# Kernel optimization log

Hardware: AMD Instinct MI355X
Metric: run time of the kernel (lower is better)

Reference implementation:

```python
import jax, jax.numpy as jnp
import numpy as np

N = 50000
E = 800000
IN_CH = 256
OUT_CH = 64   # per-head channels (PyG out_channels)
HEADS = 4
NEG_SLOPE = 0.2


def setup_inputs() -> dict:
    key = jax.random.key(0)
    k = jax.random.split(key, 8)
    x = jax.random.normal(k[0], (N, IN_CH), dtype=jnp.float32)
    edge_index = jax.random.randint(k[1], (2, E), 0, N, dtype=jnp.int64)
    # GATConv parameters
    W = jax.random.normal(k[2], (IN_CH, HEADS * OUT_CH), dtype=jnp.float32) * (1.0 / np.sqrt(IN_CH))
    att_src = jax.random.normal(k[3], (HEADS, OUT_CH), dtype=jnp.float32) * 0.1
    att_dst = jax.random.normal(k[4], (HEADS, OUT_CH), dtype=jnp.float32) * 0.1
    bias = jnp.zeros((OUT_CH,), dtype=jnp.float32)
    # residual linear (bias=False)
    W_res = jax.random.normal(k[5], (IN_CH, OUT_CH), dtype=jnp.float32) * (1.0 / np.sqrt(IN_CH))
    return {"x": x, "edge_index": edge_index, "W": W, "att_src": att_src,
            "att_dst": att_dst, "bias": bias, "W_res": W_res}


def _gat_forward(x, edge_index, W, att_src, att_dst, bias, W_res):
    # residual branch
    x_res = x @ W_res                                   # [N, OUT_CH]

    # node transform: [N, H, C]
    xw = (x @ W).reshape(N, HEADS, OUT_CH)
    # per-node attention logits, [N, H]
    a_src = jnp.einsum('nhc,hc->nh', xw, att_src)
    a_dst = jnp.einsum('nhc,hc->nh', xw, att_dst)

    # add self-loops (PyG GATConv default add_self_loops=True)
    loops = jnp.arange(N, dtype=edge_index.dtype)
    src = jnp.concatenate([edge_index[0], loops])       # [E+N]
    dst = jnp.concatenate([edge_index[1], loops])       # [E+N]

    # per-edge logits + leaky relu, [E+N, H]
    alpha = jax.nn.leaky_relu(a_src[src] + a_dst[dst], NEG_SLOPE)

    # segment softmax over destination nodes
    m = jax.ops.segment_max(alpha, dst, num_segments=N)    # [N, H]
    e = jnp.exp(alpha - m[dst])
    denom = jax.ops.segment_sum(e, dst, num_segments=N)    # [N, H]
    a = e / denom[dst]                                     # [E+N, H]
    # (dropout p=0.1 on attention coeffs is identity in eval mode)

    # weighted scatter-aggregate: [N, H, C]
    msgs = xw[src] * a[:, :, None]
    out = jax.ops.segment_sum(msgs, dst, num_segments=N)

    # concat=False -> mean over heads, then bias
    x_conv = out.mean(axis=1) + bias                     # [N, OUT_CH]
    return jax.nn.relu(x_conv + x_res)


def reference(x, edge_index, W, att_src, att_dst, bias, W_res):
    return _gat_forward(x, edge_index, W, att_src, att_dst, bias, W_res)
```

## Files before the change

### kernel.cpp

```cpp
#include <hip/hip_runtime.h>
#include <math.h>

#define N_NODES 50000
#define N_EDGES 800000
#define IN_CH   256
#define OUT_CH  64
#define HEADS   4
#define NEG_SLOPE 0.2f
#define NCOLS   320
#define NTILES  20
#define NKK     8
#define PACK_BLOCKS 40
#define GEMM_BLOCKS 782
#define NBINS   391
#define P1_BLOCKS 256
#define EPB     3125
#define AGG_BLOCKS 6250
#define STASH_CAP 2816

typedef __attribute__((ext_vector_type(8))) short short8;
typedef __attribute__((ext_vector_type(4))) float f32x4;

__device__ __forceinline__ float lrelu(float v) {
    return v > 0.f ? v : NEG_SLOPE * v;
}
__device__ __forceinline__ unsigned bf16_rne(float f) {
    unsigned u = __float_as_uint(f);
    return (u + 0x7FFFu + ((u >> 16) & 1u)) >> 16;
}
__device__ __forceinline__ unsigned pack2(float lo, float hi) {
    return bf16_rne(lo) | (bf16_rne(hi) << 16);
}
__device__ __forceinline__ float bflo(unsigned u) { return __uint_as_float(u << 16); }
__device__ __forceinline__ float bfhi(unsigned u) { return __uint_as_float(u & 0xFFFF0000u); }
__device__ __forceinline__ short8 as_short8(uint4 u) {
    union { uint4 u4; short8 s8; } cv; cv.u4 = u; return cv.s8;
}

__global__ __launch_bounds__(256) void pack_B(
    const float* __restrict__ W, const float* __restrict__ Wres,
    uint4* __restrict__ Bp)
{
    const int idx  = blockIdx.x * 256 + threadIdx.x;
    const int kk   = idx / (NTILES * 64);
    const int rem  = idx - kk * (NTILES * 64);
    const int t    = rem >> 6;
    const int lane = rem & 63;
    const int colL = lane & 15, quad = lane >> 4;
    const int col  = t * 16 + colL;
    const int k0   = kk * 32 + quad * 8;
    float v[8];
    #pragma unroll
    for (int j = 0; j < 8; ++j) {
        const int k = k0 + j;
        v[j] = (col < IN_CH) ? W[(size_t)k * IN_CH + col]
                             : Wres[(size_t)k * OUT_CH + (col - IN_CH)];
    }
    uint4 u;
    u.x = pack2(v[0], v[1]); u.y = pack2(v[2], v[3]);
    u.z = pack2(v[4], v[5]); u.w = pack2(v[6], v[7]);
    Bp[(kk * NTILES + t) * 64 + lane] = u;
}

__global__ __launch_bounds__(256) void gemm_hist(
    const float* __restrict__ x, const uint4* __restrict__ Bp,
    uint2* __restrict__ xw2, float* __restrict__ xres,
    const int* __restrict__ ei, int* __restrict__ M,
    const float* __restrict__ attS, const float* __restrict__ attD,
    float* __restrict__ asrc, float* __restrict__ adst)
{
    __shared__ uint4 Alds[4 * NKK * 64];
    __shared__ float logS[64][HEADS];
    __shared__ float logD[64][HEADS];

    if (blockIdx.x >= GEMM_BLOCKS) {
        const int blk = blockIdx.x - GEMM_BLOCKS;
        int* lh = (int*)Alds;
        for (int b = threadIdx.x; b < NBINS; b += 256) lh[b] = 0;
        __syncthreads();
        const int e0 = blk * EPB;
        #pragma unroll
        for (int r = 0; r < 13; ++r) {
            const int idx = (r << 8) + threadIdx.x;
            if (idx < EPB)
                atomicAdd(&lh[ei[N_EDGES + e0 + idx] >> 7], 1);
        }
        __syncthreads();
        for (int b = threadIdx.x; b < NBINS; b += 256)
            M[(size_t)b * P1_BLOCKS + blk] = lh[b];
        return;
    }

    const int tid = threadIdx.x;
    const int n0  = blockIdx.x * 64;

    logS[tid >> 2][tid & 3] = 0.f;
    logD[tid >> 2][tid & 3] = 0.f;

    #pragma unroll
    for (int i = 0; i < 8; ++i) {
        const int e    = i * 256 + tid;
        const int g    = e >> 9;
        const int kk   = (e >> 6) & 7;
        const int lane = e & 63;
        const int cL   = lane & 15, qd = lane >> 4;
        const int row  = n0 + g * 16 + cL;
        const int k0   = kk * 32 + qd * 8;
        uint4 u = make_uint4(0u, 0u, 0u, 0u);
        if (row < N_NODES) {
            const float4 a = *reinterpret_cast<const float4*>(x + (size_t)row * IN_CH + k0);
            const float4 b = *reinterpret_cast<const float4*>(x + (size_t)row * IN_CH + k0 + 4);
            u.x = pack2(a.x, a.y); u.y = pack2(a.z, a.w);
            u.z = pack2(b.x, b.y); u.w = pack2(b.z, b.w);
        }
        Alds[(g * NKK + kk) * 64 + lane] = u;
    }
    __syncthreads();

    const int lane = tid & 63;
    const int wv   = tid >> 6;
    const int colL = lane & 15, quad = lane >> 4;

    f32x4 acc[4][5];
    #pragma unroll
    for (int rg = 0; rg < 4; ++rg)
        #pragma unroll
        for (int j = 0; j < 5; ++j) acc[rg][j] = (f32x4){0.f, 0.f, 0.f, 0.f};

    for (int kk = 0; kk < NKK; ++kk) {
        uint4 bu[5];
        #pragma unroll
        for (int j = 0; j < 5; ++j)
            bu[j] = Bp[(kk * NTILES + j * 4 + wv) * 64 + lane];
        #pragma unroll
        for (int rg = 0; rg < 4; ++rg) {
            const short8 a = as_short8(Alds[(rg * NKK + kk) * 64 + lane]);
            #pragma unroll
            for (int j = 0; j < 5; ++j)
                acc[rg][j] = __builtin_amdgcn_mfma_f32_16x16x32_bf16(
                    a, as_short8(bu[j]), acc[rg][j], 0, 0, 0);
        }
    }

    #pragma unroll
    for (int rg = 0; rg < 4; ++rg) {
        #pragma unroll
        for (int r = 0; r < 4; ++r) {
            const int row = n0 + rg * 16 + quad * 4 + r;
            if (row < N_NODES) {
                xw2[(size_t)row * 64 + wv * 16 + colL] = make_uint2(
                    pack2(acc[rg][0][r], acc[rg][1][r]),
                    pack2(acc[rg][2][r], acc[rg][3][r]));
                xres[(size_t)row * OUT_CH + wv * 16 + colL] = acc[rg][4][r];
            }
        }
    }

    float aSr[HEADS], aDr[HEADS];
    #pragma unroll
    for (int h = 0; h < HEADS; ++h) {
        aSr[h] = attS[h * 64 + wv * 16 + colL];
        aDr[h] = attD[h * 64 + wv * 16 + colL];
    }
    #pragma unroll
    for (int rg = 0; rg < 4; ++rg) {
        #pragma unroll
        for (int h = 0; h < HEADS; ++h) {
            #pragma unroll
            for (int r = 0; r < 4; ++r) {
                float vS = acc[rg][h][r] * aSr[h];
                float vD = acc[rg][h][r] * aDr[h];
                #pragma unroll
                for (int m = 1; m < 16; m <<= 1) {
                    vS += __shfl_xor(vS, m);
                    vD += __shfl_xor(vD, m);
                }
                if (colL == 0) {
                    atomicAdd(&logS[rg * 16 + quad * 4 + r][h], vS);
                    atomicAdd(&logD[rg * 16 + quad * 4 + r][h], vD);
                }
            }
        }
    }
    __syncthreads();
    {
        const int rl = tid >> 2, h = tid & 3;
        const int row = n0 + rl;
        if (row < N_NODES) {
            asrc[(size_t)row * HEADS + h] = logS[rl][h];
            adst[(size_t)row * HEADS + h] = logD[rl][h];
        }
    }
}

__global__ __launch_bounds__(256) void binscan_M(
    int* __restrict__ M, int* __restrict__ binCnt)
{
    __shared__ int ws[4];
    const int t = threadIdx.x, lane = t & 63, w = t >> 6;
    const int b = blockIdx.x;
    const int v = M[(size_t)b * P1_BLOCKS + t];
    int sc = v;
    #pragma unroll
    for (int off = 1; off < 64; off <<= 1) {
        const int n = __shfl_up(sc, off);
        if (lane >= off) sc += n;
    }
    if (lane == 63) ws[w] = sc;
    __syncthreads();
    int prefix = 0;
    for (int j = 0; j < w; ++j) prefix += ws[j];
    M[(size_t)b * P1_BLOCKS + t] = prefix + sc - v;
    if (t == 255) binCnt[b] = prefix + sc;
}

__global__ __launch_bounds__(256) void part_mid(
    const int* __restrict__ ei, const int* __restrict__ M,
    const int* __restrict__ binCnt, unsigned* __restrict__ mid)
{
    __shared__ int bc[NBINS];
    __shared__ int bs[NBINS];
    __shared__ int baseL[NBINS];
    __shared__ int lh[NBINS];
    __shared__ int ws[4];
    const int t = threadIdx.x, lane = t & 63, wv = t >> 6;
    const int blk = blockIdx.x;

    for (int b = t; b < NBINS; b += 256) {
        bc[b] = binCnt[b];
        baseL[b] = M[(size_t)b * P1_BLOCKS + blk];
        lh[b] = 0;
    }
    __syncthreads();

    int tot0;
    {
        const int v = bc[t];
        int sc = v;
        #pragma unroll
        for (int off = 1; off < 64; off <<= 1) {
            const int n = __shfl_up(sc, off);
            if (lane >= off) sc += n;
        }
        if (lane == 63) ws[wv] = sc;
        __syncthreads();
        int prefix = 0;
        for (int j = 0; j < wv; ++j) prefix += ws[j];
        bs[t] = prefix + sc - v;
        tot0 = ws[0] + ws[1] + ws[2] + ws[3];
        __syncthreads();
    }
    {
        const int i2 = 256 + t;
        const int v = (i2 < NBINS) ? bc[i2] : 0;
        int sc = v;
        #pragma unroll
        for (int off = 1; off < 64; off <<= 1) {
            const int n = __shfl_up(sc, off);
            if (lane >= off) sc += n;
        }
        if (lane == 63) ws[wv] = sc;
        __syncthreads();
        int prefix = 0;
        for (int j = 0; j < wv; ++j) prefix += ws[j];
        if (i2 < NBINS) bs[i2] = tot0 + prefix + sc - v;
        __syncthreads();
    }
    for (int b = t; b < NBINS; b += 256) baseL[b] += bs[b];
    __syncthreads();

    const int e0 = blk * EPB;
    #pragma unroll
    for (int r = 0; r < 13; ++r) {
        const int idx = (r << 8) + t;
        if (idx < EPB) {
            const int e = e0 + idx;
            const int d = ei[N_EDGES + e];
            const int b = d >> 7;
            const int pos = atomicAdd(&lh[b], 1);
            mid[baseL[b] + pos] = ((unsigned)(d & 127) << 17) | (unsigned)ei[e];
        }
    }
}

__global__ __launch_bounds__(256) void scatter_fine2(
    const unsigned* __restrict__ mid, const int* __restrict__ binCnt,
    int* __restrict__ cnt, int* __restrict__ lscan, int* __restrict__ esrc)
{
    __shared__ int ws[4];
    __shared__ int c128[128];
    __shared__ int o128[128];
    __shared__ int w0tot;
    __shared__ unsigned stash[STASH_CAP];
    const int t = threadIdx.x, lane = t & 63, wv = t >> 6;
    const int b = blockIdx.x;

    int acc = 0;
    for (int j = t; j < NBINS; j += 256)
        if (j < b) acc += binCnt[j];
    #pragma unroll
    for (int off = 32; off >= 1; off >>= 1) acc += __shfl_xor(acc, off);
    if (lane == 0) ws[wv] = acc;
    if (t < 128) c128[t] = 0;
    __syncthreads();
    const int base = ws[0] + ws[1] + ws[2] + ws[3];
    const int n = binCnt[b];

    for (int i = t; i < n; i += 256) {
        const unsigned m = mid[base + i];
        if (i < STASH_CAP) stash[i] = m;
        atomicAdd(&c128[m >> 17], 1);
    }
    __syncthreads();

    if (t < 128) {
        const int v = c128[t];
        int sc = v;
        #pragma unroll
        for (int off = 1; off < 64; off <<= 1) {
            const int nn = __shfl_up(sc, off);
            if (lane >= off) sc += nn;
        }
        if (t == 63) w0tot = sc;
        __syncthreads();
        const int ex = sc - v + (t >= 64 ? w0tot : 0);
        o128[t] = ex;
        const int d = (b << 7) + t;
        if (d < N_NODES) {
            cnt[d] = v;
            lscan[d] = base + ex;
        }
        c128[t] = 0;
    } else {
        __syncthreads();
    }
    __syncthreads();

    for (int i = t; i < n; i += 256) {
        const unsigned m = (i < STASH_CAP) ? stash[i] : mid[base + i];
        const int dlo = (int)(m >> 17);
        const int pos = atomicAdd(&c128[dlo], 1);
        esrc[base + o128[dlo] + pos] = (int)(m & 0x1FFFFu);
    }
}

__global__ __launch_bounds__(256) void aggregate(
    const int* __restrict__ esrc, const int* __restrict__ lscan,
    const int* __restrict__ cnt,
    const float* __restrict__ asrc, const float* __restrict__ adst,
    const uint2* __restrict__ xw2, const float* __restrict__ xres,
    const float* __restrict__ bias, float* __restrict__ out,
    const int d0)
{
    __shared__ float4 wbuf[4][64];
    __shared__ int    sbuf[4][64];
    const int t = threadIdx.x;
    const int lane = t & 63;
    const int wv   = t >> 6;

    const int d = d0 + blockIdx.x * 4 + wv;
    const int row = lscan[d];
    const int deg = cnt[d];
    const float4 ad = *reinterpret_cast<const float4*>(adst + (size_t)d * 4);
    const char* xwB = (const char*)xw2;
    const int laneB = lane << 3;

    float dn0 = 0.f, dn1 = 0.f, dn2 = 0.f, dn3 = 0.f;
    float ac0 = 0.f, ac1 = 0.f, ac2 = 0.f, ac3 = 0.f;

    for (int base = 0; base < deg; base += 64) {
        const int m = min(64, deg - base);
        if (lane < m) {
            const int s = esrc[row + base + lane];
            const float4 as = *reinterpret_cast<const float4*>(asrc + (size_t)s * 4);
            const float e0 = __expf(lrelu(as.x + ad.x));
            const float e1 = __expf(lrelu(as.y + ad.y));
            const float e2 = __expf(lrelu(as.z + ad.z));
            const float e3 = __expf(lrelu(as.w + ad.w));
            dn0 += e0; dn1 += e1; dn2 += e2; dn3 += e3;
            wbuf[wv][lane] = make_float4(e0, e1, e2, e3);
            sbuf[wv][lane] = s << 9;
        }
        int j = 0;
        for (; j + 4 <= m; j += 4) {
            uint2 v0 = *(const uint2*)(xwB + sbuf[wv][j]     + laneB);
            uint2 v1 = *(const uint2*)(xwB + sbuf[wv][j + 1] + laneB);
            uint2 v2 = *(const uint2*)(xwB + sbuf[wv][j + 2] + laneB);
            uint2 v3 = *(const uint2*)(xwB + sbuf[wv][j + 3] + laneB);
            {
                const float4 w = wbuf[wv][j];
                ac0 = fmaf(w.x, bflo(v0.x), ac0); ac1 = fmaf(w.y, bfhi(v0.x), ac1);
                ac2 = fmaf(w.z, bflo(v0.y), ac2); ac3 = fmaf(w.w, bfhi(v0.y), ac3);
            }
            {
                const float4 w = wbuf[wv][j + 1];
                ac0 = fmaf(w.x, bflo(v1.x), ac0); ac1 = fmaf(w.y, bfhi(v1.x), ac1);
                ac2 = fmaf(w.z, bflo(v1.y), ac2); ac3 = fmaf(w.w, bfhi(v1.y), ac3);
            }
            {
                const float4 w = wbuf[wv][j + 2];
                ac0 = fmaf(w.x, bflo(v2.x), ac0); ac1 = fmaf(w.y, bfhi(v2.x), ac1);
                ac2 = fmaf(w.z, bflo(v2.y), ac2); ac3 = fmaf(w.w, bfhi(v2.y), ac3);
            }
            {
                const float4 w = wbuf[wv][j + 3];
                ac0 = fmaf(w.x, bflo(v3.x), ac0); ac1 = fmaf(w.y, bfhi(v3.x), ac1);
                ac2 = fmaf(w.z, bflo(v3.y), ac2); ac3 = fmaf(w.w, bfhi(v3.y), ac3);
            }
        }
        for (; j < m; ++j) {
            const float4 w = wbuf[wv][j];
            const uint2 v = *(const uint2*)(xwB + sbuf[wv][j] + laneB);
            ac0 = fmaf(w.x, bflo(v.x), ac0);
            ac1 = fmaf(w.y, bfhi(v.x), ac1);
            ac2 = fmaf(w.z, bflo(v.y), ac2);
            ac3 = fmaf(w.w, bfhi(v.y), ac3);
        }
    }

    #pragma unroll
    for (int off = 32; off >= 1; off >>= 1) {
        dn0 += __shfl_xor(dn0, off);
        dn1 += __shfl_xor(dn1, off);
        dn2 += __shfl_xor(dn2, off);
        dn3 += __shfl_xor(dn3, off);
    }
    const float4 asd = *reinterpret_cast<const float4*>(asrc + (size_t)d * 4);
    const float s0 = __expf(lrelu(asd.x + ad.x));
    const float s1 = __expf(lrelu(asd.y + ad.y));
    const float s2 = __expf(lrelu(asd.z + ad.z));
    const float s3 = __expf(lrelu(asd.w + ad.w));
    const uint2 u = xw2[(size_t)d * 64 + lane];
    ac0 = fmaf(s0, bflo(u.x), ac0); ac1 = fmaf(s1, bfhi(u.x), ac1);
    ac2 = fmaf(s2, bflo(u.y), ac2); ac3 = fmaf(s3, bfhi(u.y), ac3);
    const float i0 = 0.25f / (dn0 + s0);
    const float i1 = 0.25f / (dn1 + s1);
    const float i2 = 0.25f / (dn2 + s2);
    const float i3 = 0.25f / (dn3 + s3);
    const float v = ac0 * i0 + ac1 * i1 + ac2 * i2 + ac3 * i3
                  + bias[lane] + xres[(size_t)d * OUT_CH + lane];
    out[(size_t)d * OUT_CH + lane] = fmaxf(v, 0.f);
}

extern "C" void kernel_launch(void* const* d_in, const int* in_sizes, int n_in,
                              void* d_out, int out_size, void* d_ws, size_t ws_size,
                              hipStream_t stream) {
    const float* x    = (const float*)d_in[0];
    const int*   ei   = (const int*)d_in[1];
    const float* W    = (const float*)d_in[2];
    const float* attS = (const float*)d_in[3];
    const float* attD = (const float*)d_in[4];
    const float* bias = (const float*)d_in[5];
    const float* Wres = (const float*)d_in[6];
    float* out = (float*)d_out;

    char* p = (char*)d_ws;
    uint4*    Bp      = (uint4*)p;    p += (size_t)NKK * NTILES * 64 * 16;
    uint2*    xw2     = (uint2*)p;    p += (size_t)N_NODES * 64 * 8;
    float*    xres    = (float*)p;    p += (size_t)N_NODES * OUT_CH * 4;
    float*    asrc    = (float*)p;    p += (size_t)N_NODES * HEADS * 4;
    float*    adst    = (float*)p;    p += (size_t)N_NODES * HEADS * 4;
    int*      M       = (int*)p;      p += (size_t)NBINS * P1_BLOCKS * 4;
    int*      binCnt  = (int*)p;      p += 512 * 4;
    int*      cnt     = (int*)p;      p += (size_t)N_NODES * 4;
    int*      lscan   = (int*)p;      p += (size_t)N_NODES * 4;
    unsigned* mid     = (unsigned*)p; p += (size_t)N_EDGES * 4;
    int*      esrc    = (int*)p;      p += (size_t)N_EDGES * 4;

    pack_B<<<PACK_BLOCKS, 256, 0, stream>>>(W, Wres, Bp);
    gemm_hist<<<GEMM_BLOCKS + P1_BLOCKS, 256, 0, stream>>>(
        x, Bp, xw2, xres, ei, M, attS, attD, asrc, adst);
    binscan_M<<<NBINS, 256, 0, stream>>>(M, binCnt);
    part_mid<<<P1_BLOCKS, 256, 0, stream>>>(ei, M, binCnt, mid);
    scatter_fine2<<<NBINS, 256, 0, stream>>>(mid, binCnt, cnt, lscan, esrc);
    aggregate<<<AGG_BLOCKS, 256, 0, stream>>>(
        esrc, lscan, cnt, asrc, adst, xw2, xres, bias, out, 0);
    aggregate<<<AGG_BLOCKS, 256, 0, stream>>>(
        esrc, lscan, cnt, asrc, adst, xw2, xres, bias, out, 25000);
}
```

Measured before the change: 237.5 us.

## Restructure GEMM so each wave owns 16 rows across all 320 columns

The fused GEMM previously staged a 64-row bf16 A tile in LDS and split the 320 output columns across waves, so attention logits had to be combined through shared-memory atomics after a barrier. Now each wave loads its own 16 rows of x straight from global memory into registers and computes all 20 column tiles. That removes the LDS staging, both block barriers and the shared atomics, and lets the asrc/adst logits be written as float4 after in-wave shuffles. The cost is 80 accumulator registers per lane and each wave re-reading all of B from global or L2. Separately, the two half-sized aggregate launches become one launch covering all 50000 nodes.

```diff
diff --git a/kernel.cpp b/kernel.cpp
--- a/kernel.cpp
+++ b/kernel.cpp
@@ -15,7 +15,7 @@
 #define NBINS   391
 #define P1_BLOCKS 256
 #define EPB     3125
-#define AGG_BLOCKS 6250
+#define AGG_BLOCKS 12500
 #define STASH_CAP 2816
 
 typedef __attribute__((ext_vector_type(8))) short short8;
@@ -69,13 +69,10 @@
     const float* __restrict__ attS, const float* __restrict__ attD,
     float* __restrict__ asrc, float* __restrict__ adst)
 {
-    __shared__ uint4 Alds[4 * NKK * 64];
-    __shared__ float logS[64][HEADS];
-    __shared__ float logD[64][HEADS];
+    __shared__ int lh[NBINS];
 
     if (blockIdx.x >= GEMM_BLOCKS) {
         const int blk = blockIdx.x - GEMM_BLOCKS;
-        int* lh = (int*)Alds;
         for (int b = threadIdx.x; b < NBINS; b += 256) lh[b] = 0;
         __syncthreads();
         const int e0 = blk * EPB;
@@ -91,104 +88,90 @@
         return;
     }
 
-    const int tid = threadIdx.x;
-    const int n0  = blockIdx.x * 64;
-
-    logS[tid >> 2][tid & 3] = 0.f;
-    logD[tid >> 2][tid & 3] = 0.f;
-
-    #pragma unroll
-    for (int i = 0; i < 8; ++i) {
-        const int e    = i * 256 + tid;
-        const int g    = e >> 9;
-        const int kk   = (e >> 6) & 7;
-        const int lane = e & 63;
-        const int cL   = lane & 15, qd = lane >> 4;
-        const int row  = n0 + g * 16 + cL;
-        const int k0   = kk * 32 + qd * 8;
-        uint4 u = make_uint4(0u, 0u, 0u, 0u);
-        if (row < N_NODES) {
-            const float4 a = *reinterpret_cast<const float4*>(x + (size_t)row * IN_CH + k0);
-            const float4 b = *reinterpret_cast<const float4*>(x + (size_t)row * IN_CH + k0 + 4);
-            u.x = pack2(a.x, a.y); u.y = pack2(a.z, a.w);
-            u.z = pack2(b.x, b.y); u.w = pack2(b.z, b.w);
-        }
-        Alds[(g * NKK + kk) * 64 + lane] = u;
-    }
-    __syncthreads();
-
+    const int tid  = threadIdx.x;
     const int lane = tid & 63;
     const int wv   = tid >> 6;
-    const int colL = lane & 15, quad = lane >> 4;
-
-    f32x4 acc[4][5];
-    #pragma unroll
-    for (int rg = 0; rg < 4; ++rg)
-        #pragma unroll
-        for (int j = 0; j < 5; ++j) acc[rg][j] = (f32x4){0.f, 0.f, 0.f, 0.f};
+    const int cL   = lane & 15, qd = lane >> 4;
+    const int n0   = blockIdx.x * 64;
+    const int arow = n0 + wv * 16 + cL;
+    const bool rowOK = arow < N_NODES;
+    const float* xrow = x + (size_t)arow * IN_CH + qd * 8;
+
+    f32x4 acc[NTILES];
+    #pragma unroll
+    for (int j = 0; j < NTILES; ++j) acc[j] = (f32x4){0.f, 0.f, 0.f, 0.f};
 
     for (int kk = 0; kk < NKK; ++kk) {
-        uint4 bu[5];
-        #pragma unroll
-        for (int j = 0; j < 5; ++j)
-            bu[j] = Bp[(kk * NTILES + j * 4 + wv) * 64 + lane];
-        #pragma unroll
-        for (int rg = 0; rg < 4; ++rg) {
-            const short8 a = as_short8(Alds[(rg * NKK + kk) * 64 + lane]);
+        uint4 a = make_uint4(0u, 0u, 0u, 0u);
+        if (rowOK) {
+            const float4 p = *reinterpret_cast<const float4*>(xrow + kk * 32);
+            const float4 q = *reinterpret_cast<const float4*>(xrow + kk * 32 + 4);
+            a.x = pack2(p.x, p.y); a.y = pack2(p.z, p.w);
+            a.z = pack2(q.x, q.y); a.w = pack2(q.z, q.w);
+        }
+        const short8 af = as_short8(a);
+        #pragma unroll
+        for (int jc = 0; jc < 5; ++jc) {
+            uint4 bu[4];
             #pragma unroll
-            for (int j = 0; j < 5; ++j)
-                acc[rg][j] = __builtin_amdgcn_mfma_f32_16x16x32_bf16(
-                    a, as_short8(bu[j]), acc[rg][j], 0, 0, 0);
-        }
-    }
-
-    #pragma unroll
-    for (int rg = 0; rg < 4; ++rg) {
-        #pragma unroll
-        for (int r = 0; r < 4; ++r) {
-            const int row = n0 + rg * 16 + quad * 4 + r;
-            if (row < N_NODES) {
-                xw2[(size_t)row * 64 + wv * 16 + colL] = make_uint2(
-                    pack2(acc[rg][0][r], acc[rg][1][r]),
-                    pack2(acc[rg][2][r], acc[rg][3][r]));
-                xres[(size_t)row * OUT_CH + wv * 16 + colL] = acc[rg][4][r];
-            }
-        }
-    }
-
-    float aSr[HEADS], aDr[HEADS];
+            for (int u = 0; u < 4; ++u)
+                bu[u] = Bp[(kk * NTILES + jc * 4 + u) * 64 + lane];
+            #pragma unroll
+            for (int u = 0; u < 4; ++u)
+                acc[jc * 4 + u] = __builtin_amdgcn_mfma_f32_16x16x32_bf16(
+                    af, as_short8(bu[u]), acc[jc * 4 + u], 0, 0, 0);
+        }
+    }
+
+    float vS[16], vD[16];
+    #pragma unroll
+    for (int i = 0; i < 16; ++i) { vS[i] = 0.f; vD[i] = 0.f; }
     #pragma unroll
     for (int h = 0; h < HEADS; ++h) {
-        aSr[h] = attS[h * 64 + wv * 16 + colL];
-        aDr[h] = attD[h * 64 + wv * 16 + colL];
-    }
-    #pragma unroll
-    for (int rg = 0; rg < 4; ++rg) {
-        #pragma unroll
-        for (int h = 0; h < HEADS; ++h) {
+        #pragma unroll
+        for (int s = 0; s < 4; ++s) {
+            const float aSv = attS[h * 64 + s * 16 + cL];
+            const float aDv = attD[h * 64 + s * 16 + cL];
+            const f32x4 t = acc[h * 4 + s];
             #pragma unroll
             for (int r = 0; r < 4; ++r) {
-                float vS = acc[rg][h][r] * aSr[h];
-                float vD = acc[rg][h][r] * aDr[h];
-                #pragma unroll
-                for (int m = 1; m < 16; m <<= 1) {
-                    vS += __shfl_xor(vS, m);
-                    vD += __shfl_xor(vD, m);
-                }
-                if (colL == 0) {
-                    atomicAdd(&logS[rg * 16 + quad * 4 + r][h], vS);
-                    atomicAdd(&logD[rg * 16 + quad * 4 + r][h], vD);
-                }
-            }
-        }
-    }
-    __syncthreads();
-    {
-        const int rl = tid >> 2, h = tid & 3;
-        const int row = n0 + rl;
+                vS[h * 4 + r] = fmaf(t[r], aSv, vS[h * 4 + r]);
+                vD[h * 4 + r] = fmaf(t[r], aDv, vD[h * 4 + r]);
+            }
+        }
+    }
+    #pragma unroll
+    for (int i = 0; i < 16; ++i) {
+        #pragma unroll
+        for (int off = 1; off < 16; off <<= 1) {
+            vS[i] += __shfl_xor(vS[i], off);
+            vD[i] += __shfl_xor(vD[i], off);
+        }
+    }
+    if (cL == 0) {
+        #pragma unroll
+        for (int r = 0; r < 4; ++r) {
+            const int row = n0 + wv * 16 + qd * 4 + r;
+            if (row < N_NODES) {
+                *reinterpret_cast<float4*>(asrc + (size_t)row * 4) =
+                    make_float4(vS[r], vS[4 + r], vS[8 + r], vS[12 + r]);
+                *reinterpret_cast<float4*>(adst + (size_t)row * 4) =
+                    make_float4(vD[r], vD[4 + r], vD[8 + r], vD[12 + r]);
+            }
+        }
+    }
+
+    #pragma unroll
+    for (int r = 0; r < 4; ++r) {
+        const int row = n0 + wv * 16 + qd * 4 + r;
         if (row < N_NODES) {
-            asrc[(size_t)row * HEADS + h] = logS[rl][h];
-            adst[(size_t)row * HEADS + h] = logD[rl][h];
+            #pragma unroll
+            for (int s = 0; s < 4; ++s) {
+                xw2[(size_t)row * 64 + s * 16 + cL] = make_uint2(
+                    pack2(acc[0 * 4 + s][r], acc[1 * 4 + s][r]),
+                    pack2(acc[2 * 4 + s][r], acc[3 * 4 + s][r]));
+                xres[(size_t)row * OUT_CH + s * 16 + cL] = acc[16 + s][r];
+            }
         }
     }
 }
@@ -349,8 +332,7 @@
     const int* __restrict__ cnt,
     const float* __restrict__ asrc, const float* __restrict__ adst,
     const uint2* __restrict__ xw2, const float* __restrict__ xres,
-    const float* __restrict__ bias, float* __restrict__ out,
-    const int d0)
+    const float* __restrict__ bias, float* __restrict__ out)
 {
     __shared__ float4 wbuf[4][64];
     __shared__ int    sbuf[4][64];
@@ -358,7 +340,7 @@
     const int lane = t & 63;
     const int wv   = t >> 6;
 
-    const int d = d0 + blockIdx.x * 4 + wv;
+    const int d = blockIdx.x * 4 + wv;
     const int row = lscan[d];
     const int deg = cnt[d];
     const float4 ad = *reinterpret_cast<const float4*>(adst + (size_t)d * 4);
@@ -474,7 +456,5 @@
     part_mid<<<P1_BLOCKS, 256, 0, stream>>>(ei, M, binCnt, mid);
     scatter_fine2<<<NBINS, 256, 0, stream>>>(mid, binCnt, cnt, lscan, esrc);
     aggregate<<<AGG_BLOCKS, 256, 0, stream>>>(
-        esrc, lscan, cnt, asrc, adst, xw2, xres, bias, out, 0);
-    aggregate<<<AGG_BLOCKS, 256, 0, stream>>>(
-        esrc, lscan, cnt, asrc, adst, xw2, xres, bias, out, 25000);
-}
+        esrc, lscan, cnt, asrc, adst, xw2, xres, bias, out);
+}
```

Result: slower. 248.0 us (+4.4%).

## Split histogram from GEMM, enlarge GEMM tile to 128 rows, merge aggregate launches

Applied to the files above, without the earlier changes.

Moves the edge histogram out of the fused GEMM launch into its own kernel. The GEMM now uses 512-thread blocks covering 128 rows, so each B fragment load from global memory is shared across twice as many rows. The two half-range aggregate launches are merged into a single launch with twice the blocks, which removes one launch. The trade-off is an extra kernel launch for the histogram, the loss of overlap between histogram and GEMM blocks, and higher LDS use per GEMM block.

```diff
diff --git a/kernel.cpp b/kernel.cpp
--- a/kernel.cpp
+++ b/kernel.cpp
@@ -11,11 +11,11 @@
 #define NTILES  20
 #define NKK     8
 #define PACK_BLOCKS 40
-#define GEMM_BLOCKS 782
+#define GEMM_BLOCKS 391
 #define NBINS   391
 #define P1_BLOCKS 256
 #define EPB     3125
-#define AGG_BLOCKS 6250
+#define AGG_BLOCKS 12500
 #define STASH_CAP 2816
 
 typedef __attribute__((ext_vector_type(8))) short short8;
@@ -62,44 +62,44 @@
     Bp[(kk * NTILES + t) * 64 + lane] = u;
 }
 
-__global__ __launch_bounds__(256) void gemm_hist(
+__global__ __launch_bounds__(256) void hist_part(
+    const int* __restrict__ ei, int* __restrict__ M)
+{
+    __shared__ int lh[NBINS];
+    const int blk = blockIdx.x;
+    for (int b = threadIdx.x; b < NBINS; b += 256) lh[b] = 0;
+    __syncthreads();
+    const int e0 = blk * EPB;
+    #pragma unroll
+    for (int r = 0; r < 13; ++r) {
+        const int idx = (r << 8) + threadIdx.x;
+        if (idx < EPB)
+            atomicAdd(&lh[ei[N_EDGES + e0 + idx] >> 7], 1);
+    }
+    __syncthreads();
+    for (int b = threadIdx.x; b < NBINS; b += 256)
+        M[(size_t)b * P1_BLOCKS + blk] = lh[b];
+}
+
+__global__ __launch_bounds__(512) void gemm_xform(
     const float* __restrict__ x, const uint4* __restrict__ Bp,
     uint2* __restrict__ xw2, float* __restrict__ xres,
-    const int* __restrict__ ei, int* __restrict__ M,
     const float* __restrict__ attS, const float* __restrict__ attD,
     float* __restrict__ asrc, float* __restrict__ adst)
 {
-    __shared__ uint4 Alds[4 * NKK * 64];
-    __shared__ float logS[64][HEADS];
-    __shared__ float logD[64][HEADS];
-
-    if (blockIdx.x >= GEMM_BLOCKS) {
-        const int blk = blockIdx.x - GEMM_BLOCKS;
-        int* lh = (int*)Alds;
-        for (int b = threadIdx.x; b < NBINS; b += 256) lh[b] = 0;
-        __syncthreads();
-        const int e0 = blk * EPB;
-        #pragma unroll
-        for (int r = 0; r < 13; ++r) {
-            const int idx = (r << 8) + threadIdx.x;
-            if (idx < EPB)
-                atomicAdd(&lh[ei[N_EDGES + e0 + idx] >> 7], 1);
-        }
-        __syncthreads();
-        for (int b = threadIdx.x; b < NBINS; b += 256)
-            M[(size_t)b * P1_BLOCKS + blk] = lh[b];
-        return;
-    }
+    __shared__ uint4 Alds[8 * NKK * 64];
+    __shared__ float logS[128][HEADS];
+    __shared__ float logD[128][HEADS];
 
     const int tid = threadIdx.x;
-    const int n0  = blockIdx.x * 64;
+    const int n0  = blockIdx.x * 128;
 
     logS[tid >> 2][tid & 3] = 0.f;
     logD[tid >> 2][tid & 3] = 0.f;
 
     #pragma unroll
     for (int i = 0; i < 8; ++i) {
-        const int e    = i * 256 + tid;
+        const int e    = i * 512 + tid;
         const int g    = e >> 9;
         const int kk   = (e >> 6) & 7;
         const int lane = e & 63;
@@ -118,7 +118,9 @@
     __syncthreads();
 
     const int lane = tid & 63;
-    const int wv   = tid >> 6;
+    const int w    = tid >> 6;
+    const int q    = w & 3;
+    const int rh   = w >> 2;
     const int colL = lane & 15, quad = lane >> 4;
 
     f32x4 acc[4][5];
@@ -131,10 +133,10 @@
         uint4 bu[5];
         #pragma unroll
         for (int j = 0; j < 5; ++j)
-            bu[j] = Bp[(kk * NTILES + j * 4 + wv) * 64 + lane];
+            bu[j] = Bp[(kk * NTILES + j * 4 + q) * 64 + lane];
         #pragma unroll
         for (int rg = 0; rg < 4; ++rg) {
-            const short8 a = as_short8(Alds[(rg * NKK + kk) * 64 + lane]);
+            const short8 a = as_short8(Alds[((rh * 4 + rg) * NKK + kk) * 64 + lane]);
             #pragma unroll
             for (int j = 0; j < 5; ++j)
                 acc[rg][j] = __builtin_amdgcn_mfma_f32_16x16x32_bf16(
@@ -146,12 +148,12 @@
     for (int rg = 0; rg < 4; ++rg) {
         #pragma unroll
         for (int r = 0; r < 4; ++r) {
-            const int row = n0 + rg * 16 + quad * 4 + r;
+            const int row = n0 + (rh * 4 + rg) * 16 + quad * 4 + r;
             if (row < N_NODES) {
-                xw2[(size_t)row * 64 + wv * 16 + colL] = make_uint2(
+                xw2[(size_t)row * 64 + q * 16 + colL] = make_uint2(
                     pack2(acc[rg][0][r], acc[rg][1][r]),
                     pack2(acc[rg][2][r], acc[rg][3][r]));
-                xres[(size_t)row * OUT_CH + wv * 16 + colL] = acc[rg][4][r];
+                xres[(size_t)row * OUT_CH + q * 16 + colL] = acc[rg][4][r];
             }
         }
     }
@@ -159,8 +161,8 @@
     float aSr[HEADS], aDr[HEADS];
     #pragma unroll
     for (int h = 0; h < HEADS; ++h) {
-        aSr[h] = attS[h * 64 + wv * 16 + colL];
-        aDr[h] = attD[h * 64 + wv * 16 + colL];
+        aSr[h] = attS[h * 64 + q * 16 + colL];
+        aDr[h] = attD[h * 64 + q * 16 + colL];
     }
     #pragma unroll
     for (int rg = 0; rg < 4; ++rg) {
@@ -176,8 +178,9 @@
                     vD += __shfl_xor(vD, m);
                 }
                 if (colL == 0) {
-                    atomicAdd(&logS[rg * 16 + quad * 4 + r][h], vS);
-                    atomicAdd(&logD[rg * 16 + quad * 4 + r][h], vD);
+                    const int rl = (rh * 4 + rg) * 16 + quad * 4 + r;
+                    atomicAdd(&logS[rl][h], vS);
+                    atomicAdd(&logD[rl][h], vD);
                 }
             }
         }
@@ -349,8 +352,7 @@
     const int* __restrict__ cnt,
     const float* __restrict__ asrc, const float* __restrict__ adst,
     const uint2* __restrict__ xw2, const float* __restrict__ xres,
-    const float* __restrict__ bias, float* __restrict__ out,
-    const int d0)
+    const float* __restrict__ bias, float* __restrict__ out)
 {
     __shared__ float4 wbuf[4][64];
     __shared__ int    sbuf[4][64];
@@ -358,7 +360,7 @@
     const int lane = t & 63;
     const int wv   = t >> 6;
 
-    const int d = d0 + blockIdx.x * 4 + wv;
+    const int d = blockIdx.x * 4 + wv;
     const int row = lscan[d];
     const int deg = cnt[d];
     const float4 ad = *reinterpret_cast<const float4*>(adst + (size_t)d * 4);
@@ -468,13 +470,12 @@
     int*      esrc    = (int*)p;      p += (size_t)N_EDGES * 4;
 
     pack_B<<<PACK_BLOCKS, 256, 0, stream>>>(W, Wres, Bp);
-    gemm_hist<<<GEMM_BLOCKS + P1_BLOCKS, 256, 0, stream>>>(
-        x, Bp, xw2, xres, ei, M, attS, attD, asrc, adst);
+    hist_part<<<P1_BLOCKS, 256, 0, stream>>>(ei, M);
+    gemm_xform<<<GEMM_BLOCKS, 512, 0, stream>>>(
+        x, Bp, xw2, xres, attS, attD, asrc, adst);
     binscan_M<<<NBINS, 256, 0, stream>>>(M, binCnt);
     part_mid<<<P1_BLOCKS, 256, 0, stream>>>(ei, M, binCnt, mid);
     scatter_fine2<<<NBINS, 256, 0, stream>>>(mid, binCnt, cnt, lscan, esrc);
     aggregate<<<AGG_BLOCKS, 256, 0, stream>>>(
-        esrc, lscan, cnt, asrc, adst, xw2, xres, bias, out, 0);
-    aggregate<<<AGG_BLOCKS, 256, 0, stream>>>(
-        esrc, lscan, cnt, asrc, adst, xw2, xres, bias, out, 25000);
-}
+        esrc, lscan, cnt, asrc, adst, xw2, xres, bias, out);
+}
```

Measured after the change: 241.1 us. No clear change (+1.5%).

## Split GEMM into chunks co-scheduled with edge-partition kernels, merge aggregate launches

Applied to the files above, without the earlier changes.

The node GEMM is split into three chunks whose blocks are fused into the same launches as the histogram scan, the coarse partition and the fine scatter. Pack_B is merged with the histogram, so the latency-bound sorting stages run alongside GEMM work instead of serially. The histogram and partition stages now use 1024 blocks of about 782 edges instead of 256 blocks of 3125. The two aggregate launches are collapsed into one. The price is larger shared-memory footprints in the mixed kernels, which may lower occupancy, plus a bigger M matrix and scan.

```diff
diff --git a/kernel.cpp b/kernel.cpp
--- a/kernel.cpp
+++ b/kernel.cpp
@@ -13,10 +13,13 @@
 #define PACK_BLOCKS 40
 #define GEMM_BLOCKS 782
 #define NBINS   391
-#define P1_BLOCKS 256
-#define EPB     3125
-#define AGG_BLOCKS 6250
+#define H_BLOCKS 1024
+#define EPB1    782
+#define AGG_BLOCKS 12500
 #define STASH_CAP 2816
+#define CHUNK_A 301
+#define CHUNK_B 301
+#define CHUNK_C 180
 
 typedef __attribute__((ext_vector_type(8))) short short8;
 typedef __attribute__((ext_vector_type(4))) float f32x4;
@@ -37,62 +40,14 @@
     union { uint4 u4; short8 s8; } cv; cv.u4 = u; return cv.s8;
 }
 
-__global__ __launch_bounds__(256) void pack_B(
-    const float* __restrict__ W, const float* __restrict__ Wres,
-    uint4* __restrict__ Bp)
+__device__ __forceinline__ void gemm_body(
+    const int n0, const float* __restrict__ x, const uint4* __restrict__ Bp,
+    uint2* __restrict__ xw2, float* __restrict__ xres,
+    const float* __restrict__ attS, const float* __restrict__ attD,
+    float* __restrict__ asrc, float* __restrict__ adst,
+    uint4* Alds, float (*logS)[HEADS], float (*logD)[HEADS])
 {
-    const int idx  = blockIdx.x * 256 + threadIdx.x;
-    const int kk   = idx / (NTILES * 64);
-    const int rem  = idx - kk * (NTILES * 64);
-    const int t    = rem >> 6;
-    const int lane = rem & 63;
-    const int colL = lane & 15, quad = lane >> 4;
-    const int col  = t * 16 + colL;
-    const int k0   = kk * 32 + quad * 8;
-    float v[8];
-    #pragma unroll
-    for (int j = 0; j < 8; ++j) {
-        const int k = k0 + j;
-        v[j] = (col < IN_CH) ? W[(size_t)k * IN_CH + col]
-                             : Wres[(size_t)k * OUT_CH + (col - IN_CH)];
-    }
-    uint4 u;
-    u.x = pack2(v[0], v[1]); u.y = pack2(v[2], v[3]);
-    u.z = pack2(v[4], v[5]); u.w = pack2(v[6], v[7]);
-    Bp[(kk * NTILES + t) * 64 + lane] = u;
-}
-
-__global__ __launch_bounds__(256) void gemm_hist(
-    const float* __restrict__ x, const uint4* __restrict__ Bp,
-    uint2* __restrict__ xw2, float* __restrict__ xres,
-    const int* __restrict__ ei, int* __restrict__ M,
-    const float* __restrict__ attS, const float* __restrict__ attD,
-    float* __restrict__ asrc, float* __restrict__ adst)
-{
-    __shared__ uint4 Alds[4 * NKK * 64];
-    __shared__ float logS[64][HEADS];
-    __shared__ float logD[64][HEADS];
-
-    if (blockIdx.x >= GEMM_BLOCKS) {
-        const int blk = blockIdx.x - GEMM_BLOCKS;
-        int* lh = (int*)Alds;
-        for (int b = threadIdx.x; b < NBINS; b += 256) lh[b] = 0;
-        __syncthreads();
-        const int e0 = blk * EPB;
-        #pragma unroll
-        for (int r = 0; r < 13; ++r) {
-            const int idx = (r << 8) + threadIdx.x;
-            if (idx < EPB)
-                atomicAdd(&lh[ei[N_EDGES + e0 + idx] >> 7], 1);
-        }
-        __syncthreads();
-        for (int b = threadIdx.x; b < NBINS; b += 256)
-            M[(size_t)b * P1_BLOCKS + blk] = lh[b];
-        return;
-    }
-
     const int tid = threadIdx.x;
-    const int n0  = blockIdx.x * 64;
 
     logS[tid >> 2][tid & 3] = 0.f;
     logD[tid >> 2][tid & 3] = 0.f;
@@ -193,155 +148,247 @@
     }
 }
 
-__global__ __launch_bounds__(256) void binscan_M(
+__global__ __launch_bounds__(256) void prep(
+    const float* __restrict__ W, const float* __restrict__ Wres,
+    uint4* __restrict__ Bp, const int* __restrict__ ei, int* __restrict__ M)
+{
+    __shared__ int lh[NBINS];
+    const int t = threadIdx.x;
+
+    if (blockIdx.x < PACK_BLOCKS) {
+        const int idx  = blockIdx.x * 256 + t;
+        const int kk   = idx / (NTILES * 64);
+        const int rem  = idx - kk * (NTILES * 64);
+        const int tt   = rem >> 6;
+        const int lane = rem & 63;
+        const int colL = lane & 15, quad = lane >> 4;
+        const int col  = tt * 16 + colL;
+        const int k0   = kk * 32 + quad * 8;
+        float v[8];
+        #pragma unroll
+        for (int j = 0; j < 8; ++j) {
+            const int k = k0 + j;
+            v[j] = (col < IN_CH) ? W[(size_t)k * IN_CH + col]
+                                 : Wres[(size_t)k * OUT_CH + (col - IN_CH)];
+        }
+        uint4 u;
+        u.x = pack2(v[0], v[1]); u.y = pack2(v[2], v[3]);
+        u.z = pack2(v[4], v[5]); u.w = pack2(v[6], v[7]);
+        Bp[(kk * NTILES + tt) * 64 + lane] = u;
+        return;
+    }
+
+    const int blk = blockIdx.x - PACK_BLOCKS;
+    for (int b = t; b < NBINS; b += 256) lh[b] = 0;
+    __syncthreads();
+    const int e0 = blk * EPB1;
+    #pragma unroll
+    for (int r = 0; r < 4; ++r) {
+        const int idx = (r << 8) + t;
+        const int e = e0 + idx;
+        if (idx < EPB1 && e < N_EDGES)
+            atomicAdd(&lh[ei[N_EDGES + e] >> 7], 1);
+    }
+    __syncthreads();
+    for (int b = t; b < NBINS; b += 256)
+        M[(size_t)b * H_BLOCKS + blk] = lh[b];
+}
+
+__global__ __launch_bounds__(256) void scan_gemmA(
+    const float* __restrict__ x, const uint4* __restrict__ Bp,
+    uint2* __restrict__ xw2, float* __restrict__ xres,
+    const float* __restrict__ attS, const float* __restrict__ attD,
+    float* __restrict__ asrc, float* __restrict__ adst,
     int* __restrict__ M, int* __restrict__ binCnt)
 {
-    __shared__ int ws[4];
-    const int t = threadIdx.x, lane = t & 63, w = t >> 6;
-    const int b = blockIdx.x;
-    const int v = M[(size_t)b * P1_BLOCKS + t];
-    int sc = v;
-    #pragma unroll
-    for (int off = 1; off < 64; off <<= 1) {
-        const int n = __shfl_up(sc, off);
-        if (lane >= off) sc += n;
-    }
-    if (lane == 63) ws[w] = sc;
-    __syncthreads();
-    int prefix = 0;
-    for (int j = 0; j < w; ++j) prefix += ws[j];
-    M[(size_t)b * P1_BLOCKS + t] = prefix + sc - v;
-    if (t == 255) binCnt[b] = prefix + sc;
-}
-
-__global__ __launch_bounds__(256) void part_mid(
+    __shared__ uint4 Alds[4 * NKK * 64];
+    __shared__ float logS[64][HEADS];
+    __shared__ float logD[64][HEADS];
+    const int t = threadIdx.x, lane = t & 63, wv = t >> 6;
+
+    if (blockIdx.x < NBINS) {
+        int* ws = (int*)Alds;
+        const int b = blockIdx.x;
+        int carry = 0;
+        for (int c = 0; c < 4; ++c) {
+            const size_t off = (size_t)b * H_BLOCKS + (c << 8) + t;
+            const int v = M[off];
+            int sc = v;
+            #pragma unroll
+            for (int o = 1; o < 64; o <<= 1) {
+                const int n = __shfl_up(sc, o);
+                if (lane >= o) sc += n;
+            }
+            if (lane == 63) ws[wv] = sc;
+            __syncthreads();
+            int prefix = 0;
+            for (int j = 0; j < wv; ++j) prefix += ws[j];
+            M[off] = carry + prefix + sc - v;
+            const int tot = ws[0] + ws[1] + ws[2] + ws[3];
+            __syncthreads();
+            carry += tot;
+        }
+        if (t == 0) binCnt[b] = carry;
+        return;
+    }
+    gemm_body((blockIdx.x - NBINS) * 64,
+              x, Bp, xw2, xres, attS, attD, asrc, adst, Alds, logS, logD);
+}
+
+__global__ __launch_bounds__(256) void part_gemmB(
+    const float* __restrict__ x, const uint4* __restrict__ Bp,
+    uint2* __restrict__ xw2, float* __restrict__ xres,
+    const float* __restrict__ attS, const float* __restrict__ attD,
+    float* __restrict__ asrc, float* __restrict__ adst,
     const int* __restrict__ ei, const int* __restrict__ M,
     const int* __restrict__ binCnt, unsigned* __restrict__ mid)
 {
-    __shared__ int bc[NBINS];
-    __shared__ int bs[NBINS];
-    __shared__ int baseL[NBINS];
-    __shared__ int lh[NBINS];
-    __shared__ int ws[4];
+    __shared__ uint4 Alds[4 * NKK * 64];
+    __shared__ float logS[64][HEADS];
+    __shared__ float logD[64][HEADS];
     const int t = threadIdx.x, lane = t & 63, wv = t >> 6;
-    const int blk = blockIdx.x;
-
-    for (int b = t; b < NBINS; b += 256) {
-        bc[b] = binCnt[b];
-        baseL[b] = M[(size_t)b * P1_BLOCKS + blk];
-        lh[b] = 0;
-    }
-    __syncthreads();
-
-    int tot0;
-    {
-        const int v = bc[t];
-        int sc = v;
-        #pragma unroll
-        for (int off = 1; off < 64; off <<= 1) {
-            const int n = __shfl_up(sc, off);
-            if (lane >= off) sc += n;
-        }
-        if (lane == 63) ws[wv] = sc;
+
+    if (blockIdx.x < H_BLOCKS) {
+        int* bc    = (int*)Alds;
+        int* bs    = bc + 392;
+        int* baseL = bs + 392;
+        int* lh    = baseL + 392;
+        int* ws    = lh + 392;
+        const int blk = blockIdx.x;
+
+        for (int b = t; b < NBINS; b += 256) {
+            bc[b] = binCnt[b];
+            baseL[b] = M[(size_t)b * H_BLOCKS + blk];
+            lh[b] = 0;
+        }
         __syncthreads();
-        int prefix = 0;
-        for (int j = 0; j < wv; ++j) prefix += ws[j];
-        bs[t] = prefix + sc - v;
-        tot0 = ws[0] + ws[1] + ws[2] + ws[3];
+
+        int tot0;
+        {
+            const int v = bc[t];
+            int sc = v;
+            #pragma unroll
+            for (int o = 1; o < 64; o <<= 1) {
+                const int n = __shfl_up(sc, o);
+                if (lane >= o) sc += n;
+            }
+            if (lane == 63) ws[wv] = sc;
+            __syncthreads();
+            int prefix = 0;
+            for (int j = 0; j < wv; ++j) prefix += ws[j];
+            bs[t] = prefix + sc - v;
+            tot0 = ws[0] + ws[1] + ws[2] + ws[3];
+            __syncthreads();
+        }
+        {
+            const int i2 = 256 + t;
+            const int v = (i2 < NBINS) ? bc[i2] : 0;
+            int sc = v;
+            #pragma unroll
+            for (int o = 1; o < 64; o <<= 1) {
+                const int n = __shfl_up(sc, o);
+                if (lane >= o) sc += n;
+            }
+            if (lane == 63) ws[wv] = sc;
+            __syncthreads();
+            int prefix = 0;
+            for (int j = 0; j < wv; ++j) prefix += ws[j];
+            if (i2 < NBINS) bs[i2] = tot0 + prefix + sc - v;
+            __syncthreads();
+        }
+        for (int b = t; b < NBINS; b += 256) baseL[b] += bs[b];
         __syncthreads();
-    }
-    {
-        const int i2 = 256 + t;
-        const int v = (i2 < NBINS) ? bc[i2] : 0;
-        int sc = v;
-        #pragma unroll
-        for (int off = 1; off < 64; off <<= 1) {
-            const int n = __shfl_up(sc, off);
-            if (lane >= off) sc += n;
-        }
-        if (lane == 63) ws[wv] = sc;
-        __syncthreads();
-        int prefix = 0;
-        for (int j = 0; j < wv; ++j) prefix += ws[j];
-        if (i2 < NBINS) bs[i2] = tot0 + prefix + sc - v;
-        __syncthreads();
-    }
-    for (int b = t; b < NBINS; b += 256) baseL[b] += bs[b];
-    __syncthreads();
-
-    const int e0 = blk * EPB;
-    #pragma unroll
-    for (int r = 0; r < 13; ++r) {
-        const int idx = (r << 8) + t;
-        if (idx < EPB) {
+
+        const int e0 = blk * EPB1;
+        #pragma unroll
+        for (int r = 0; r < 4; ++r) {
+            const int idx = (r << 8) + t;
             const int e = e0 + idx;
-            const int d = ei[N_EDGES + e];
-            const int b = d >> 7;
-            const int pos = atomicAdd(&lh[b], 1);
-            mid[baseL[b] + pos] = ((unsigned)(d & 127) << 17) | (unsigned)ei[e];
-        }
-    }
-}
-
-__global__ __launch_bounds__(256) void scatter_fine2(
+            if (idx < EPB1 && e < N_EDGES) {
+                const int d = ei[N_EDGES + e];
+                const int b = d >> 7;
+                const int pos = atomicAdd(&lh[b], 1);
+                mid[baseL[b] + pos] = ((unsigned)(d & 127) << 17) | (unsigned)ei[e];
+            }
+        }
+        return;
+    }
+    gemm_body((CHUNK_A + blockIdx.x - H_BLOCKS) * 64,
+              x, Bp, xw2, xres, attS, attD, asrc, adst, Alds, logS, logD);
+}
+
+__global__ __launch_bounds__(256) void scat_gemmC(
+    const float* __restrict__ x, const uint4* __restrict__ Bp,
+    uint2* __restrict__ xw2, float* __restrict__ xres,
+    const float* __restrict__ attS, const float* __restrict__ attD,
+    float* __restrict__ asrc, float* __restrict__ adst,
     const unsigned* __restrict__ mid, const int* __restrict__ binCnt,
     int* __restrict__ cnt, int* __restrict__ lscan, int* __restrict__ esrc)
 {
-    __shared__ int ws[4];
-    __shared__ int c128[128];
-    __shared__ int o128[128];
-    __shared__ int w0tot;
-    __shared__ unsigned stash[STASH_CAP];
+    __shared__ uint4 Alds[4 * NKK * 64];
+    __shared__ float logS[64][HEADS];
+    __shared__ float logD[64][HEADS];
     const int t = threadIdx.x, lane = t & 63, wv = t >> 6;
-    const int b = blockIdx.x;
-
-    int acc = 0;
-    for (int j = t; j < NBINS; j += 256)
-        if (j < b) acc += binCnt[j];
-    #pragma unroll
-    for (int off = 32; off >= 1; off >>= 1) acc += __shfl_xor(acc, off);
-    if (lane == 0) ws[wv] = acc;
-    if (t < 128) c128[t] = 0;
-    __syncthreads();
-    const int base = ws[0] + ws[1] + ws[2] + ws[3];
-    const int n = binCnt[b];
-
-    for (int i = t; i < n; i += 256) {
-        const unsigned m = mid[base + i];
-        if (i < STASH_CAP) stash[i] = m;
-        atomicAdd(&c128[m >> 17], 1);
-    }
-    __syncthreads();
-
-    if (t < 128) {
-        const int v = c128[t];
-        int sc = v;
-        #pragma unroll
-        for (int off = 1; off < 64; off <<= 1) {
-            const int nn = __shfl_up(sc, off);
-            if (lane >= off) sc += nn;
-        }
-        if (t == 63) w0tot = sc;
+
+    if (blockIdx.x < NBINS) {
+        int*      ws    = (int*)Alds;
+        int*      c128  = ws + 4;
+        int*      o128  = c128 + 128;
+        int*      w0t   = o128 + 128;
+        unsigned* stash = (unsigned*)(w0t + 4);
+        const int b = blockIdx.x;
+
+        int acc = 0;
+        for (int j = t; j < NBINS; j += 256)
+            if (j < b) acc += binCnt[j];
+        #pragma unroll
+        for (int o = 32; o >= 1; o >>= 1) acc += __shfl_xor(acc, o);
+        if (lane == 0) ws[wv] = acc;
+        if (t < 128) c128[t] = 0;
         __syncthreads();
-        const int ex = sc - v + (t >= 64 ? w0tot : 0);
-        o128[t] = ex;
-        const int d = (b << 7) + t;
-        if (d < N_NODES) {
-            cnt[d] = v;
-            lscan[d] = base + ex;
-        }
-        c128[t] = 0;
-    } else {
+        const int base = ws[0] + ws[1] + ws[2] + ws[3];
+        const int n = binCnt[b];
+
+        for (int i = t; i < n; i += 256) {
+            const unsigned m = mid[base + i];
+            if (i < STASH_CAP) stash[i] = m;
+            atomicAdd(&c128[m >> 17], 1);
+        }
         __syncthreads();
-    }
-    __syncthreads();
-
-    for (int i = t; i < n; i += 256) {
-        const unsigned m = (i < STASH_CAP) ? stash[i] : mid[base + i];
-        const int dlo = (int)(m >> 17);
-        const int pos = atomicAdd(&c128[dlo], 1);
-        esrc[base + o128[dlo] + pos] = (int)(m & 0x1FFFFu);
-    }
+
+        if (t < 128) {
+            const int v = c128[t];
+            int sc = v;
+            #pragma unroll
+            for (int o = 1; o < 64; o <<= 1) {
+                const int nn = __shfl_up(sc, o);
+                if (lane >= o) sc += nn;
+            }
+            if (t == 63) *w0t = sc;
+            __syncthreads();
+            const int ex = sc - v + (t >= 64 ? *w0t : 0);
+            o128[t] = ex;
+            const int d = (b << 7) + t;
+            if (d < N_NODES) {
+                cnt[d] = v;
+                lscan[d] = base + ex;
+            }
+            c128[t] = 0;
+        } else {
+            __syncthreads();
+        }
+        __syncthreads();
+
+        for (int i = t; i < n; i += 256) {
+            const unsigned m = (i < STASH_CAP) ? stash[i] : mid[base + i];
+            const int dlo = (int)(m >> 17);
+            const int pos = atomicAdd(&c128[dlo], 1);
+            esrc[base + o128[dlo] + pos] = (int)(m & 0x1FFFFu);
+        }
+        return;
+    }
+    gemm_body((CHUNK_A + CHUNK_B + blockIdx.x - NBINS) * 64,
+              x, Bp, xw2, xres, attS, attD, asrc, adst, Alds, logS, logD);
 }
 
 __global__ __launch_bounds__(256) void aggregate(
@@ -349,8 +396,7 @@
     const int* __restrict__ cnt,
     const float* __restrict__ asrc, const float* __restrict__ adst,
     const uint2* __restrict__ xw2, const float* __restrict__ xres,
-    const float* __restrict__ bias, float* __restrict__ out,
-    const int d0)
+    const float* __restrict__ bias, float* __restrict__ out)
 {
     __shared__ float4 wbuf[4][64];
     __shared__ int    sbuf[4][64];
@@ -358,7 +404,7 @@
     const int lane = t & 63;
     const int wv   = t >> 6;
 
-    const int d = d0 + blockIdx.x * 4 + wv;
+    const int d = blockIdx.x * 4 + wv;
     const int row = lscan[d];
     const int deg = cnt[d];
     const float4 ad = *reinterpret_cast<const float4*>(adst + (size_t)d * 4);
@@ -460,21 +506,20 @@
     float*    xres    = (float*)p;    p += (size_t)N_NODES * OUT_CH * 4;
     float*    asrc    = (float*)p;    p += (size_t)N_NODES * HEADS * 4;
     float*    adst    = (float*)p;    p += (size_t)N_NODES * HEADS * 4;
-    int*      M       = (int*)p;      p += (size_t)NBINS * P1_BLOCKS * 4;
+    int*      M       = (int*)p;      p += (size_t)NBINS * H_BLOCKS * 4;
     int*      binCnt  = (int*)p;      p += 512 * 4;
     int*      cnt     = (int*)p;      p += (size_t)N_NODES * 4;
     int*      lscan   = (int*)p;      p += (size_t)N_NODES * 4;
     unsigned* mid     = (unsigned*)p; p += (size_t)N_EDGES * 4;
     int*      esrc    = (int*)p;      p += (size_t)N_EDGES * 4;
 
-    pack_B<<<PACK_BLOCKS, 256, 0, stream>>>(W, Wres, Bp);
-    gemm_hist<<<GEMM_BLOCKS + P1_BLOCKS, 256, 0, stream>>>(
-        x, Bp, xw2, xres, ei, M, attS, attD, asrc, adst);
-    binscan_M<<<NBINS, 256, 0, stream>>>(M, binCnt);
-    part_mid<<<P1_BLOCKS, 256, 0, stream>>>(ei, M, binCnt, mid);
-    scatter_fine2<<<NBINS, 256, 0, stream>>>(mid, binCnt, cnt, lscan, esrc);
+    prep<<<PACK_BLOCKS + H_BLOCKS, 256, 0, stream>>>(W, Wres, Bp, ei, M);
+    scan_gemmA<<<NBINS + CHUNK_A, 256, 0, stream>>>(
+        x, Bp, xw2, xres, attS, attD, asrc, adst, M, binCnt);
+    part_gemmB<<<H_BLOCKS + CHUNK_B, 256, 0, stream>>>(
+        x, Bp, xw2, xres, attS, attD, asrc, adst, ei, M, binCnt, mid);
+    scat_gemmC<<<NBINS + CHUNK_C, 256, 0, stream>>>(
+        x, Bp, xw2, xres, attS, attD, asrc, adst, mid, binCnt, cnt, lscan, esrc);
     aggregate<<<AGG_BLOCKS, 256, 0, stream>>>(
-        esrc, lscan, cnt, asrc, adst, xw2, xres, bias, out, 0);
-    aggregate<<<AGG_BLOCKS, 256, 0, stream>>>(
-        esrc, lscan, cnt, asrc, adst, xw2, xres, bias, out, 25000);
-}
+        esrc, lscan, cnt, asrc, adst, xw2, xres, bias, out);
+}
```

Result: slower. 263.5 us (+11.0%).
